# Kernel tuning notes

Measured on AMD Instinct MI355X. Metric: run time of the kernel, lower is better.

The kernel has to match this reference:

```python
import jax, jax.numpy as jnp
import numpy as np

NUM_EMBEDDINGS = 1024
EMBEDDING_DIM = 256
COMMITMENT_COST = 0.25
DECAY = 0.99
EPSILON = 1e-05


def setup_inputs() -> dict:
    key = jax.random.key(0)
    k1, k2, k3 = jax.random.split(key, 3)
    z = jax.random.normal(k1, (32, EMBEDDING_DIM, 32, 32), dtype=jnp.float32)
    codebook = jax.random.normal(k2, (NUM_EMBEDDINGS, EMBEDDING_DIM), dtype=jnp.float32)
    ema_cluster_size = jnp.zeros((NUM_EMBEDDINGS,), dtype=jnp.float32)
    ema_dw = jax.random.normal(k3, (NUM_EMBEDDINGS, EMBEDDING_DIM), dtype=jnp.float32)
    return {"z": z, "codebook": codebook, "ema_cluster_size": ema_cluster_size, "ema_dw": ema_dw}


def reference(z, codebook, ema_cluster_size, ema_dw):
    K, D = codebook.shape
    # (B,C,H,W) -> (B,H,W,C)
    zp = jnp.transpose(z, (0, 2, 3, 1))
    z_flat = zp.reshape(-1, D)  # [N, D]
    N = z_flat.shape[0]

    # squared L2 distances to each code: [N, K]
    distances = (jnp.sum(z_flat ** 2, axis=1, keepdims=True)
                 + jnp.sum(codebook ** 2, axis=1)
                 - 2.0 * z_flat @ codebook.T)
    idx = jnp.argmin(distances, axis=1)  # [N]

    quantized = codebook[idx].reshape(zp.shape)  # [B,H,W,C]

    # training-mode EMA codebook update (one-hot scatter expressed as segment sums)
    counts = jax.ops.segment_sum(jnp.ones((N,), z_flat.dtype), idx, num_segments=K)  # encodings.sum(0)
    dw = jax.ops.segment_sum(z_flat, idx, num_segments=K)                            # encodings.T @ z_flat
    new_cluster_size = ema_cluster_size * DECAY + (1.0 - DECAY) * counts
    new_ema_dw = ema_dw * DECAY + (1.0 - DECAY) * dw
    n = jnp.sum(new_cluster_size)
    cluster_size = (new_cluster_size + EPSILON) / (n + K * EPSILON) * n
    new_codebook = new_ema_dw / cluster_size[:, None]

    commitment_loss = jnp.mean((zp - jax.lax.stop_gradient(quantized)) ** 2)
    loss = COMMITMENT_COST * commitment_loss

    # straight-through estimator
    quantized_st = zp + jax.lax.stop_gradient(quantized - zp)

    avg_probs = counts / N
    perplexity = jnp.exp(-jnp.sum(avg_probs * jnp.log(avg_probs + 1e-10)))

    quantized_out = jnp.transpose(quantized_st, (0, 3, 1, 2))  # back to (B,C,H,W)
    return (quantized_out, loss, perplexity, new_codebook, new_cluster_size, new_ema_dw)
```

## Files before the change

### kernel.cpp

```cpp
#include <hip/hip_runtime.h>
#include <cfloat>
#include <cstdint>

#define B_BATCH 32
#define D_DIM   256
#define HW      1024
#define N_POS   32768
#define K_CODES 1024
#define DECAY_F   0.99f
#define ONE_M_DECAY 0.01f
#define EPS_F   1e-5f

#define OUT_Q    0
#define OUT_LOSS 8388608
#define OUT_PERP 8388609
#define OUT_CB   8388610
#define OUT_NCS  8650754
#define OUT_EDW  8651778


#define WS_COUNTS  0
#define WS_ZNORM   4096
#define WS_BSUM    4100
#define WS_MEMSET  4104
#define WS_CBNORM  4352
#define WS_OFFS    8448
#define WS_CURSOR  12544
#define WS_IDX     16640
#define WS_SORTED  147712
#define WS_CBHI    278784
#define WS_CBLO    803072
#define WS_PART    1327360
#define WS_SCODE   3424512
#define WS_TOTAL   3555584

typedef short s16x8 __attribute__((ext_vector_type(8)));
typedef float f32x4 __attribute__((ext_vector_type(4)));
typedef unsigned long long u64;

__device__ __forceinline__ ushort f2bf_rne(float x) {
    uint u = __float_as_uint(x);
    uint r = (u + 0x7FFF + ((u >> 16) & 1)) >> 16;
    return (ushort)r;
}
__device__ __forceinline__ float bf2f(ushort h) {
    return __uint_as_float(((uint)h) << 16);
}

__device__ __forceinline__ void gload16(const void* g, void* l) {
    __builtin_amdgcn_global_load_lds(
        (const __attribute__((address_space(1))) unsigned*)(uintptr_t)g,
        (__attribute__((address_space(3))) unsigned*)(uintptr_t)l, 16, 0, 0);
}

__global__ __launch_bounds__(256) void prep_ztrans(const float* __restrict__ z,
                                                   const float* __restrict__ cb,
                                                   ushort* __restrict__ zhi,
                                                   ushort* __restrict__ zlo,
                                                   ushort* __restrict__ cbhi,
                                                   ushort* __restrict__ cblo,
                                                   float* __restrict__ cbnorm,
                                                   float* __restrict__ znorm_acc) {
    __shared__ float Zs[32][65];
    __shared__ float red[256];
    const int tid = threadIdx.x;

    if (blockIdx.x >= 512) {
        int wave = tid >> 6;
        int lane = tid & 63;
        int k = (blockIdx.x - 512) * 4 + wave;
        float4 v = *(const float4*)&cb[(size_t)k * D_DIM + lane * 4];
        ushort4 h, l;
        h.x = f2bf_rne(v.x); l.x = f2bf_rne(v.x - bf2f(h.x));
        h.y = f2bf_rne(v.y); l.y = f2bf_rne(v.y - bf2f(h.y));
        h.z = f2bf_rne(v.z); l.z = f2bf_rne(v.z - bf2f(h.z));
        h.w = f2bf_rne(v.w); l.w = f2bf_rne(v.w - bf2f(h.w));
        *(ushort4*)&cbhi[(size_t)k * D_DIM + lane * 4] = h;
        *(ushort4*)&cblo[(size_t)k * D_DIM + lane * 4] = l;
        float s = v.x * v.x + v.y * v.y + v.z * v.z + v.w * v.w;
        #pragma unroll
        for (int off = 32; off >= 1; off >>= 1) s += __shfl_xor(s, off);
        if (lane == 0) cbnorm[k] = s;
        return;
    }

    const int n0  = blockIdx.x * 64;
    const int b   = n0 >> 10;
    const int hw0 = n0 & 1023;
    const float* zb = z + (size_t)b * (D_DIM * HW) + hw0;

    const int zn = tid & 63;
    const int zdb = (tid >> 6) * 8;
    const int n  = tid >> 2;
    const int dq = tid & 3;
    float zsum = 0.f;

    for (int d0 = 0; d0 < D_DIM; d0 += 32) {
        __syncthreads();
        #pragma unroll
        for (int j = 0; j < 8; ++j)
            Zs[zdb + j][zn] = zb[(size_t)(d0 + zdb + j) * HW + zn];
        __syncthreads();
        s16x8 hv, lv;
        #pragma unroll
        for (int j = 0; j < 8; ++j) {
            float f = Zs[dq * 8 + j][n];
            zsum += f * f;
            ushort hb = f2bf_rne(f);
            ushort lb = f2bf_rne(f - bf2f(hb));
            hv[j] = (short)hb;
            lv[j] = (short)lb;
        }
        *(s16x8*)&zhi[(size_t)(n0 + n) * D_DIM + d0 + dq * 8] = hv;
        *(s16x8*)&zlo[(size_t)(n0 + n) * D_DIM + d0 + dq * 8] = lv;
    }
    red[tid] = zsum;
    __syncthreads();
    for (int s2 = 128; s2 >= 1; s2 >>= 1) {
        if (tid < s2) red[tid] += red[tid + s2];
        __syncthreads();
    }
    if (tid == 0) atomicAdd(znorm_acc, red[0]);
}

__global__ __launch_bounds__(256) void argmin_gemm(const ushort* __restrict__ cbhi,
                                                   const ushort* __restrict__ cblo,
                                                   const ushort* __restrict__ zhi,
                                                   const ushort* __restrict__ zlo,
                                                   const float* __restrict__ cbnorm,
                                                   u64* __restrict__ partial) {
    __shared__ ushort lds[16384];
    __shared__ u64 kred[128][2];

    const int tid  = threadIdx.x;
    const int wave = tid >> 6;
    const int lane = tid & 63;
    const int col  = lane & 15;
    const int lg   = lane >> 4;
    const int blk = blockIdx.x;
    const int mt = (blk >> 3) & 7;
    const int pt = (blk & 7) | ((blk >> 6) << 3);
    const int ch = wave & 1;
    const int ph = wave >> 1;

    const int r0  = tid >> 2;
    const int dch = (tid & 3) ^ ((r0 >> 1) & 3);
    const size_t eA0 = (size_t)(mt * 128 + r0) * D_DIM + dch * 8;
    const size_t eB0 = (size_t)(pt * 128 + r0) * D_DIM + dch * 8;
    const int ldsw = wave * 512;

    const int swz = (lg ^ ((col >> 1) & 3)) * 8;
    const int soffA = (ch * 64 + col) * 32 + swz;
    const int soffB = (ph * 64 + col) * 32 + swz;

    f32x4 acc[4][4];
    #pragma unroll
    for (int mi = 0; mi < 4; ++mi)
        #pragma unroll
        for (int ni = 0; ni < 4; ++ni) acc[mi][ni] = {0.f, 0.f, 0.f, 0.f};

    for (int s8 = 0; s8 < 8; ++s8) {
        const int d0 = s8 * 32;
        __syncthreads();
        gload16(cbhi + eA0 + d0,            &lds[0     + ldsw]);
        gload16(cbhi + eA0 + 64 * 256 + d0, &lds[2048  + ldsw]);
        gload16(cblo + eA0 + d0,            &lds[4096  + ldsw]);
        gload16(cblo + eA0 + 64 * 256 + d0, &lds[6144  + ldsw]);
        gload16(zhi  + eB0 + d0,            &lds[8192  + ldsw]);
        gload16(zhi  + eB0 + 64 * 256 + d0, &lds[10240 + ldsw]);
        gload16(zlo  + eB0 + d0,            &lds[12288 + ldsw]);
        gload16(zlo  + eB0 + 64 * 256 + d0, &lds[14336 + ldsw]);
        __syncthreads();

        s16x8 ah[4], al[4], bh[4], bl[4];
        #pragma unroll
        for (int mi = 0; mi < 4; ++mi) {
            int so = soffA + mi * 512;
            ah[mi] = *(const s16x8*)&lds[so];
            al[mi] = *(const s16x8*)&lds[4096 + so];
        }
        #pragma unroll
        for (int ni = 0; ni < 4; ++ni) {
            int so = soffB + ni * 512;
            bh[ni] = *(const s16x8*)&lds[8192 + so];
            bl[ni] = *(const s16x8*)&lds[12288 + so];
        }
        #pragma unroll
        for (int mi = 0; mi < 4; ++mi)
            #pragma unroll
            for (int ni = 0; ni < 4; ++ni) {
                acc[mi][ni] = __builtin_amdgcn_mfma_f32_16x16x32_bf16(ah[mi], bh[ni], acc[mi][ni], 0, 0, 0);
                acc[mi][ni] = __builtin_amdgcn_mfma_f32_16x16x32_bf16(ah[mi], bl[ni], acc[mi][ni], 0, 0, 0);
                acc[mi][ni] = __builtin_amdgcn_mfma_f32_16x16x32_bf16(al[mi], bh[ni], acc[mi][ni], 0, 0, 0);
            }
    }

    const int kbase = mt * 128 + ch * 64;
    u64 best[4] = {~0ull, ~0ull, ~0ull, ~0ull};
    #pragma unroll
    for (int mi = 0; mi < 4; ++mi) {
        float4 cn = *(const float4*)&cbnorm[kbase + mi * 16 + lg * 4];
        const float* cnp = (const float*)&cn;
        #pragma unroll
        for (int ni = 0; ni < 4; ++ni) {
            #pragma unroll
            for (int r = 0; r < 4; ++r) {
                float dist = cnp[r] - 2.f * acc[mi][ni][r];
                uint ub = __float_as_uint(dist);
                ub = ub ^ (uint)(((int)ub >> 31) | 0x80000000);
                u64 key = ((u64)ub << 32) | (uint)(kbase + mi * 16 + lg * 4 + r);
                if (key < best[ni]) best[ni] = key;
            }
        }
    }
    #pragma unroll
    for (int ni = 0; ni < 4; ++ni) {
        u64 o = __shfl_xor(best[ni], 16); if (o < best[ni]) best[ni] = o;
        o = __shfl_xor(best[ni], 32); if (o < best[ni]) best[ni] = o;
    }
    if (lane < 16) {
        #pragma unroll
        for (int ni = 0; ni < 4; ++ni)
            kred[ph * 64 + ni * 16 + lane][ch] = best[ni];
    }
    __syncthreads();
    if (tid < 128) {
        u64 a = kred[tid][0], b = kred[tid][1];
        partial[(size_t)(pt * 128 + tid) * 8 + mt] = a < b ? a : b;
    }
}

__global__ __launch_bounds__(256) void combine_kernel(const u64* __restrict__ partial,
                                                      int* __restrict__ idx,
                                                      float* __restrict__ counts,
                                                      float* __restrict__ bsum_acc) {
    __shared__ int hist[1024];
    __shared__ float red[256];
    const int tid = threadIdx.x;
    for (int j = tid; j < 1024; j += 256) hist[j] = 0;
    __syncthreads();
    int n = blockIdx.x * 256 + tid;
    const u64* p = partial + (size_t)n * 8;
    u64 m = p[0];
    #pragma unroll
    for (int j = 1; j < 8; ++j) { u64 v = p[j]; if (v < m) m = v; }
    int k = (int)(m & 1023u);
    idx[n] = k;
    atomicAdd(&hist[k], 1);
    uint ub = (uint)(m >> 32);
    uint u = (ub & 0x80000000u) ? (ub ^ 0x80000000u) : ~ub;
    red[tid] = __uint_as_float(u);
    __syncthreads();
    for (int s2 = 128; s2 >= 1; s2 >>= 1) {
        if (tid < s2) red[tid] += red[tid + s2];
        __syncthreads();
    }
    if (tid == 0) atomicAdd(bsum_acc, red[0]);
    for (int j = tid; j < 1024; j += 256) {
        int c = hist[j];
        if (c) atomicAdd(&counts[j], (float)c);
    }
}

__global__ __launch_bounds__(1024) void small_kernel(const float* __restrict__ ema_cs,
                                                     const float* __restrict__ counts,
                                                     const float* __restrict__ znorm,
                                                     const float* __restrict__ bsum,
                                                     float* __restrict__ out_ncs,
                                                     float* __restrict__ out_perp,
                                                     float* __restrict__ out_loss,
                                                     float* __restrict__ ntot_ws,
                                                     int* __restrict__ offsets,
                                                     int* __restrict__ cursor) {
    __shared__ float s1[1024];
    __shared__ float s2[1024];
    __shared__ int   s3[1024];
    int k = threadIdx.x;
    float cnt = counts[k];
    float ncs = ema_cs[k] * DECAY_F + ONE_M_DECAY * cnt;
    out_ncs[k] = ncs;
    float p = cnt / (float)N_POS;
    s1[k] = ncs;
    s2[k] = p * logf(p + 1e-10f);
    int c = (int)cnt;
    s3[k] = c;
    __syncthreads();
    for (int off = 1; off < 1024; off <<= 1) {
        int v = (k >= off) ? s3[k - off] : 0;
        __syncthreads();
        s3[k] += v;
        __syncthreads();
    }
    int excl = s3[k] - c;
    offsets[k] = excl;
    cursor[k] = excl;
    for (int st = 512; st >= 1; st >>= 1) {
        if (k < st) { s1[k] += s1[k + st]; s2[k] += s2[k + st]; }
        __syncthreads();
    }
    if (k == 0) {
        ntot_ws[0] = s1[0];
        out_perp[0] = expf(-s2[0]);
        out_loss[0] = 0.25f * (znorm[0] + bsum[0]) / 8388608.0f;
    }
}

__global__ __launch_bounds__(256) void scatter_kernel(const int* __restrict__ idx,
                                                      int* __restrict__ cursor,
                                                      int* __restrict__ sorted,
                                                      int* __restrict__ scode,
                                                      float* __restrict__ dw_zero) {
    __shared__ int hist[1024];
    __shared__ int base_s[1024];
    const int tid = threadIdx.x;
    {
        float4 z4 = {0.f, 0.f, 0.f, 0.f};
        size_t e = ((size_t)blockIdx.x * 256 + tid) * 8;
        *(float4*)&dw_zero[e] = z4;
        *(float4*)&dw_zero[e + 4] = z4;
    }
    for (int j = tid; j < 1024; j += 256) hist[j] = 0;
    __syncthreads();
    int n = blockIdx.x * 256 + tid;
    int k = idx[n];
    atomicAdd(&hist[k], 1);
    __syncthreads();
    for (int j = tid; j < 1024; j += 256) {
        int c = hist[j];
        if (c) base_s[j] = atomicAdd(&cursor[j], c);
        hist[j] = 0;
    }
    __syncthreads();
    int rank = atomicAdd(&hist[k], 1);
    int pos = base_s[k] + rank;
    sorted[pos] = n;
    scode[pos] = k;
}

#define DW_CHUNK 64
__global__ __launch_bounds__(256) void dw_chunk_kernel(const ushort* __restrict__ zhi,
                                                       const ushort* __restrict__ zlo,
                                                       const int* __restrict__ sorted,
                                                       const int* __restrict__ scode,
                                                       const int* __restrict__ offsets,
                                                       const float* __restrict__ counts,
                                                       float* __restrict__ dw) {
    __shared__ int sid[DW_CHUNK];
    __shared__ int sk[DW_CHUNK];
    const int tid = threadIdx.x;
    const int p0 = blockIdx.x * DW_CHUNK;
    if (tid < DW_CHUNK) {
        sid[tid] = sorted[p0 + tid];
        sk[tid]  = scode[p0 + tid];
    }
    __syncthreads();
    float acc = 0.f;
    int runstart = 0;
    #pragma unroll 4
    for (int i = 0; i < DW_CHUNK; ++i) {
        int id = sid[i];
        float zv = bf2f(zhi[(size_t)id * D_DIM + tid]) + bf2f(zlo[(size_t)id * D_DIM + tid]);
        acc += zv;
        bool end = (i == DW_CHUNK - 1) || (sk[i + 1] != sk[i]);
        if (end) {
            int k = sk[i];
            int off = offsets[k];
            int cnt = (int)counts[k];
            if (p0 + runstart == off && p0 + i == off + cnt - 1)
                dw[(size_t)k * D_DIM + tid] = acc;
            else
                atomicAdd(&dw[(size_t)k * D_DIM + tid], acc);
            acc = 0.f;
            runstart = i + 1;
        }
    }
}

__global__ __launch_bounds__(256) void fuse_lite(const float* __restrict__ cb,
                                                 const int* __restrict__ idx,
                                                 float* __restrict__ outq) {
    __shared__ float Qs[32][65];
    __shared__ int kidx[64];
    const int tid = threadIdx.x;
    const int n0  = blockIdx.x * 64;
    const int b   = n0 >> 10;
    const int hw0 = n0 & 1023;
    float* ob = outq + (size_t)b * (D_DIM * HW) + hw0;

    if (tid < 64) kidx[tid] = idx[n0 + tid];

    for (int d0 = 0; d0 < D_DIM; d0 += 32) {
        __syncthreads();
        #pragma unroll
        for (int h = 0; h < 2; ++h) {
            int s  = tid + 256 * h;
            int n  = s >> 3;
            int dq = s & 7;
            int k  = kidx[n];
            float4 q = *(const float4*)&cb[(size_t)k * D_DIM + d0 + dq * 4];
            Qs[dq * 4 + 0][n] = q.x;
            Qs[dq * 4 + 1][n] = q.y;
            Qs[dq * 4 + 2][n] = q.z;
            Qs[dq * 4 + 3][n] = q.w;
        }
        __syncthreads();
        #pragma unroll
        for (int j = 0; j < 8; ++j) {
            int v = tid + 256 * j;
            int d = v >> 6;
            int n = v & 63;
            ob[(size_t)(d0 + d) * HW + n] = Qs[d][n];
        }
    }
}

__global__ __launch_bounds__(256) void finalize_rows(const float* __restrict__ ema_dw,
                                                     const float* __restrict__ out_ncs,
                                                     const float* __restrict__ ntot_ws,
                                                     float* __restrict__ out_edw,
                                                     float* __restrict__ out_cb) {
    int k = blockIdx.x;
    int d = threadIdx.x;
    float ncs = out_ncs[k];
    float nt = ntot_ws[0];
    float csz = (ncs + EPS_F) / (nt + (float)K_CODES * EPS_F) * nt;
    size_t e = (size_t)k * D_DIM + d;
    float ed = ema_dw[e] * DECAY_F + ONE_M_DECAY * out_edw[e];
    out_edw[e] = ed;
    out_cb[e] = ed / csz;
}

extern "C" void kernel_launch(void* const* d_in, const int* in_sizes, int n_in,
                              void* d_out, int out_size, void* d_ws, size_t ws_size,
                              hipStream_t stream) {
    const float* z       = (const float*)d_in[0];
    const float* cb      = (const float*)d_in[1];
    const float* ema_cs  = (const float*)d_in[2];
    const float* ema_dw  = (const float*)d_in[3];
    float* out = (float*)d_out;

    char* ws = (char*)d_ws;
    float* ws_counts = (float*)(ws + WS_COUNTS);
    float* ws_znorm  = (float*)(ws + WS_ZNORM);
    float* ws_bsum   = (float*)(ws + WS_BSUM);
    float* ws_cbnorm = (float*)(ws + WS_CBNORM);
    int*   ws_offs   = (int*)(ws + WS_OFFS);
    int*   ws_cursor = (int*)(ws + WS_CURSOR);
    int*   ws_idx    = (int*)(ws + WS_IDX);
    int*   ws_sorted = (int*)(ws + WS_SORTED);
    ushort* ws_cbhi  = (ushort*)(ws + WS_CBHI);
    ushort* ws_cblo  = (ushort*)(ws + WS_CBLO);
    u64*   ws_part   = (u64*)(ws + WS_PART);
    int*   ws_scode  = (int*)(ws + WS_SCODE);

    ushort* zhi = (ushort*)out;
    ushort* zlo = zhi + 8388608;

    hipMemsetAsync(d_ws, 0, WS_MEMSET, stream);

    prep_ztrans<<<768, 256, 0, stream>>>(z, cb, zhi, zlo, ws_cbhi, ws_cblo,
                                         ws_cbnorm, ws_znorm);
    argmin_gemm<<<2048, 256, 0, stream>>>(ws_cbhi, ws_cblo, zhi, zlo, ws_cbnorm, ws_part);
    combine_kernel<<<N_POS / 256, 256, 0, stream>>>(ws_part, ws_idx, ws_counts, ws_bsum);
    small_kernel<<<1, 1024, 0, stream>>>(ema_cs, ws_counts, ws_znorm, ws_bsum,
                                         out + OUT_NCS, out + OUT_PERP, out + OUT_LOSS,
                                         (float*)(ws + WS_ZNORM) + 1024, ws_offs, ws_cursor);
    scatter_kernel<<<N_POS / 256, 256, 0, stream>>>(ws_idx, ws_cursor, ws_sorted,
                                                    ws_scode, out + OUT_EDW);
    dw_chunk_kernel<<<N_POS / DW_CHUNK, 256, 0, stream>>>(zhi, zlo, ws_sorted, ws_scode,
                                                          ws_offs, ws_counts, out + OUT_EDW);
    fuse_lite<<<N_POS / 64, 256, 0, stream>>>(cb, ws_idx, out + OUT_Q);
    finalize_rows<<<K_CODES, 256, 0, stream>>>(ema_dw, out + OUT_NCS,
                                               (float*)(ws + WS_ZNORM) + 1024,
                                               out + OUT_EDW, out + OUT_CB);
}
```

Before: 213.9 us.

## Fuse combine and stats into argmin GEMM via last-block tickets; merge tail kernels

Folds the argmin combine step and the single-block statistics/prefix-sum kernel into the GEMM kernel. Atomic ticket counters let the last-arriving block per position tile do the combine, and the very last block compute the scan, perplexity and loss. The quantize-output kernel and the codebook finalize kernel are merged into one launch by block index. This removes three kernel launches and their serialization gaps, at the cost of extra threadfences and atomics plus a serial tail executed by a single block inside the GEMM.

Measured after the change: 453.4 us. +111.9%, slower.

```diff
diff --git a/kernel.cpp b/kernel.cpp
--- a/kernel.cpp
+++ b/kernel.cpp
@@ -22,17 +22,20 @@
 #define WS_COUNTS  0
 #define WS_ZNORM   4096
 #define WS_BSUM    4100
-#define WS_MEMSET  4104
-#define WS_CBNORM  4352
-#define WS_OFFS    8448
-#define WS_CURSOR  12544
-#define WS_IDX     16640
-#define WS_SORTED  147712
-#define WS_CBHI    278784
-#define WS_CBLO    803072
-#define WS_PART    1327360
-#define WS_SCODE   3424512
-#define WS_TOTAL   3555584
+#define WS_DONE    4104
+#define WS_NTOT    4108
+#define WS_TICKET  4112
+#define WS_MEMSET  5136
+#define WS_CBNORM  5376
+#define WS_OFFS    9472
+#define WS_CURSOR  13568
+#define WS_IDX     17664
+#define WS_SORTED  148736
+#define WS_CBHI    279808
+#define WS_CBLO    804096
+#define WS_PART    1328384
+#define WS_SCODE   3425536
+#define WS_TOTAL   3556608
 
 typedef short s16x8 __attribute__((ext_vector_type(8)));
 typedef float f32x4 __attribute__((ext_vector_type(4)));
@@ -128,9 +131,23 @@
                                                    const ushort* __restrict__ zhi,
                                                    const ushort* __restrict__ zlo,
                                                    const float* __restrict__ cbnorm,
-                                                   u64* __restrict__ partial) {
+                                                   u64* __restrict__ partial,
+                                                   int* __restrict__ ticket,
+                                                   int* __restrict__ done_ctr,
+                                                   int* __restrict__ idx,
+                                                   float* __restrict__ counts,
+                                                   float* __restrict__ bsum_acc,
+                                                   const float* __restrict__ znorm,
+                                                   const float* __restrict__ ema_cs,
+                                                   float* __restrict__ out_ncs,
+                                                   float* __restrict__ out_perp,
+                                                   float* __restrict__ out_loss,
+                                                   float* __restrict__ ntot_ws,
+                                                   int* __restrict__ offsets,
+                                                   int* __restrict__ cursor) {
     __shared__ ushort lds[16384];
     __shared__ u64 kred[128][2];
+    __shared__ int s_last, s_vlast;
 
     const int tid  = threadIdx.x;
     const int wave = tid >> 6;
@@ -228,80 +245,96 @@
         u64 a = kred[tid][0], b = kred[tid][1];
         partial[(size_t)(pt * 128 + tid) * 8 + mt] = a < b ? a : b;
     }
-}
-
-__global__ __launch_bounds__(256) void combine_kernel(const u64* __restrict__ partial,
-                                                      int* __restrict__ idx,
-                                                      float* __restrict__ counts,
-                                                      float* __restrict__ bsum_acc) {
-    __shared__ int hist[1024];
-    __shared__ float red[256];
-    const int tid = threadIdx.x;
+
+    __threadfence();
+    __syncthreads();
+    if (tid == 0) s_last = (atomicAdd(&ticket[pt], 1) == 7);
+    __syncthreads();
+    if (!s_last) return;
+
+    __threadfence();
+    int* hist = (int*)lds;
+    float* redf = (float*)((char*)lds + 4096);
     for (int j = tid; j < 1024; j += 256) hist[j] = 0;
     __syncthreads();
-    int n = blockIdx.x * 256 + tid;
-    const u64* p = partial + (size_t)n * 8;
-    u64 m = p[0];
-    #pragma unroll
-    for (int j = 1; j < 8; ++j) { u64 v = p[j]; if (v < m) m = v; }
-    int k = (int)(m & 1023u);
-    idx[n] = k;
-    atomicAdd(&hist[k], 1);
-    uint ub = (uint)(m >> 32);
-    uint u = (ub & 0x80000000u) ? (ub ^ 0x80000000u) : ~ub;
-    red[tid] = __uint_as_float(u);
+    float bd = 0.f;
+    if (tid < 128) {
+        int n = pt * 128 + tid;
+        const u64* p = partial + (size_t)n * 8;
+        u64 m = p[0];
+        #pragma unroll
+        for (int j = 1; j < 8; ++j) { u64 v = p[j]; if (v < m) m = v; }
+        int k = (int)(m & 1023u);
+        idx[n] = k;
+        atomicAdd(&hist[k], 1);
+        uint ub = (uint)(m >> 32);
+        uint u = (ub & 0x80000000u) ? (ub ^ 0x80000000u) : ~ub;
+        bd = __uint_as_float(u);
+    }
+    redf[tid] = bd;
     __syncthreads();
     for (int s2 = 128; s2 >= 1; s2 >>= 1) {
-        if (tid < s2) red[tid] += red[tid + s2];
-        __syncthreads();
-    }
-    if (tid == 0) atomicAdd(bsum_acc, red[0]);
+        if (tid < s2) redf[tid] += redf[tid + s2];
+        __syncthreads();
+    }
+    if (tid == 0) atomicAdd(bsum_acc, redf[0]);
     for (int j = tid; j < 1024; j += 256) {
         int c = hist[j];
         if (c) atomicAdd(&counts[j], (float)c);
     }
-}
-
-__global__ __launch_bounds__(1024) void small_kernel(const float* __restrict__ ema_cs,
-                                                     const float* __restrict__ counts,
-                                                     const float* __restrict__ znorm,
-                                                     const float* __restrict__ bsum,
-                                                     float* __restrict__ out_ncs,
-                                                     float* __restrict__ out_perp,
-                                                     float* __restrict__ out_loss,
-                                                     float* __restrict__ ntot_ws,
-                                                     int* __restrict__ offsets,
-                                                     int* __restrict__ cursor) {
-    __shared__ float s1[1024];
-    __shared__ float s2[1024];
-    __shared__ int   s3[1024];
-    int k = threadIdx.x;
-    float cnt = counts[k];
-    float ncs = ema_cs[k] * DECAY_F + ONE_M_DECAY * cnt;
-    out_ncs[k] = ncs;
-    float p = cnt / (float)N_POS;
-    s1[k] = ncs;
-    s2[k] = p * logf(p + 1e-10f);
-    int c = (int)cnt;
-    s3[k] = c;
-    __syncthreads();
-    for (int off = 1; off < 1024; off <<= 1) {
-        int v = (k >= off) ? s3[k - off] : 0;
-        __syncthreads();
-        s3[k] += v;
-        __syncthreads();
-    }
-    int excl = s3[k] - c;
-    offsets[k] = excl;
-    cursor[k] = excl;
-    for (int st = 512; st >= 1; st >>= 1) {
-        if (k < st) { s1[k] += s1[k + st]; s2[k] += s2[k + st]; }
-        __syncthreads();
-    }
-    if (k == 0) {
+
+    __threadfence();
+    __syncthreads();
+    if (tid == 0) s_vlast = (atomicAdd(done_ctr, 1) == 255);
+    __syncthreads();
+    if (!s_vlast) return;
+
+    __threadfence();
+    int*   si = (int*)lds;
+    float* s1 = (float*)((char*)lds + 4096);
+    float* s2 = (float*)((char*)lds + 5120);
+    const int base = tid * 4;
+    int c4[4];
+    int ssum = 0;
+    float n1 = 0.f, n2 = 0.f;
+    #pragma unroll
+    for (int j = 0; j < 4; ++j) {
+        float cnt = counts[base + j];
+        int ci = (int)cnt;
+        c4[j] = ci;
+        ssum += ci;
+        float ncs = ema_cs[base + j] * DECAY_F + ONE_M_DECAY * cnt;
+        out_ncs[base + j] = ncs;
+        n1 += ncs;
+        float p = cnt / (float)N_POS;
+        n2 += p * logf(p + 1e-10f);
+    }
+    si[tid] = ssum;
+    __syncthreads();
+    for (int off = 1; off < 256; off <<= 1) {
+        int v = (tid >= off) ? si[tid - off] : 0;
+        __syncthreads();
+        si[tid] += v;
+        __syncthreads();
+    }
+    int run = si[tid] - ssum;
+    #pragma unroll
+    for (int j = 0; j < 4; ++j) {
+        offsets[base + j] = run;
+        cursor[base + j] = run;
+        run += c4[j];
+    }
+    s1[tid] = n1;
+    s2[tid] = n2;
+    __syncthreads();
+    for (int st = 128; st >= 1; st >>= 1) {
+        if (tid < st) { s1[tid] += s1[tid + st]; s2[tid] += s2[tid + st]; }
+        __syncthreads();
+    }
+    if (tid == 0) {
         ntot_ws[0] = s1[0];
         out_perp[0] = expf(-s2[0]);
-        out_loss[0] = 0.25f * (znorm[0] + bsum[0]) / 8388608.0f;
+        out_loss[0] = 0.25f * (znorm[0] + bsum_acc[0]) / 8388608.0f;
     }
 }
 
@@ -376,13 +409,31 @@
     }
 }
 
-__global__ __launch_bounds__(256) void fuse_lite(const float* __restrict__ cb,
-                                                 const int* __restrict__ idx,
-                                                 float* __restrict__ outq) {
+__global__ __launch_bounds__(256) void tail_kernel(const float* __restrict__ cb,
+                                                   const int* __restrict__ idx,
+                                                   const float* __restrict__ ema_dw,
+                                                   const float* __restrict__ out_ncs,
+                                                   const float* __restrict__ ntot_ws,
+                                                   float* __restrict__ out_edw,
+                                                   float* __restrict__ out_cb,
+                                                   float* __restrict__ outq) {
     __shared__ float Qs[32][65];
     __shared__ int kidx[64];
     const int tid = threadIdx.x;
-    const int n0  = blockIdx.x * 64;
+
+    if (blockIdx.x < 1024) {
+        int k = blockIdx.x;
+        float ncs = out_ncs[k];
+        float nt = ntot_ws[0];
+        float csz = (ncs + EPS_F) / (nt + (float)K_CODES * EPS_F) * nt;
+        size_t e = (size_t)k * D_DIM + tid;
+        float ed = ema_dw[e] * DECAY_F + ONE_M_DECAY * out_edw[e];
+        out_edw[e] = ed;
+        out_cb[e] = ed / csz;
+        return;
+    }
+
+    const int n0  = (blockIdx.x - 1024) * 64;
     const int b   = n0 >> 10;
     const int hw0 = n0 & 1023;
     float* ob = outq + (size_t)b * (D_DIM * HW) + hw0;
@@ -414,22 +465,6 @@
     }
 }
 
-__global__ __launch_bounds__(256) void finalize_rows(const float* __restrict__ ema_dw,
-                                                     const float* __restrict__ out_ncs,
-                                                     const float* __restrict__ ntot_ws,
-                                                     float* __restrict__ out_edw,
-                                                     float* __restrict__ out_cb) {
-    int k = blockIdx.x;
-    int d = threadIdx.x;
-    float ncs = out_ncs[k];
-    float nt = ntot_ws[0];
-    float csz = (ncs + EPS_F) / (nt + (float)K_CODES * EPS_F) * nt;
-    size_t e = (size_t)k * D_DIM + d;
-    float ed = ema_dw[e] * DECAY_F + ONE_M_DECAY * out_edw[e];
-    out_edw[e] = ed;
-    out_cb[e] = ed / csz;
-}
-
 extern "C" void kernel_launch(void* const* d_in, const int* in_sizes, int n_in,
                               void* d_out, int out_size, void* d_ws, size_t ws_size,
                               hipStream_t stream) {
@@ -443,6 +478,9 @@
     float* ws_counts = (float*)(ws + WS_COUNTS);
     float* ws_znorm  = (float*)(ws + WS_ZNORM);
     float* ws_bsum   = (float*)(ws + WS_BSUM);
+    int*   ws_done   = (int*)(ws + WS_DONE);
+    float* ws_ntot   = (float*)(ws + WS_NTOT);
+    int*   ws_ticket = (int*)(ws + WS_TICKET);
     float* ws_cbnorm = (float*)(ws + WS_CBNORM);
     int*   ws_offs   = (int*)(ws + WS_OFFS);
     int*   ws_cursor = (int*)(ws + WS_CURSOR);
@@ -460,17 +498,15 @@
 
     prep_ztrans<<<768, 256, 0, stream>>>(z, cb, zhi, zlo, ws_cbhi, ws_cblo,
                                          ws_cbnorm, ws_znorm);
-    argmin_gemm<<<2048, 256, 0, stream>>>(ws_cbhi, ws_cblo, zhi, zlo, ws_cbnorm, ws_part);
-    combine_kernel<<<N_POS / 256, 256, 0, stream>>>(ws_part, ws_idx, ws_counts, ws_bsum);
-    small_kernel<<<1, 1024, 0, stream>>>(ema_cs, ws_counts, ws_znorm, ws_bsum,
-                                         out + OUT_NCS, out + OUT_PERP, out + OUT_LOSS,
-                                         (float*)(ws + WS_ZNORM) + 1024, ws_offs, ws_cursor);
+    argmin_gemm<<<2048, 256, 0, stream>>>(ws_cbhi, ws_cblo, zhi, zlo, ws_cbnorm,
+                                          ws_part, ws_ticket, ws_done,
+                                          ws_idx, ws_counts, ws_bsum, ws_znorm,
+                                          ema_cs, out + OUT_NCS, out + OUT_PERP,
+                                          out + OUT_LOSS, ws_ntot, ws_offs, ws_cursor);
     scatter_kernel<<<N_POS / 256, 256, 0, stream>>>(ws_idx, ws_cursor, ws_sorted,
                                                     ws_scode, out + OUT_EDW);
     dw_chunk_kernel<<<N_POS / DW_CHUNK, 256, 0, stream>>>(zhi, zlo, ws_sorted, ws_scode,
                                                           ws_offs, ws_counts, out + OUT_EDW);
-    fuse_lite<<<N_POS / 64, 256, 0, stream>>>(cb, ws_idx, out + OUT_Q);
-    finalize_rows<<<K_CODES, 256, 0, stream>>>(ema_dw, out + OUT_NCS,
-                                               (float*)(ws + WS_ZNORM) + 1024,
-                                               out + OUT_EDW, out + OUT_CB);
-}
+    tail_kernel<<<1536, 256, 0, stream>>>(cb, ws_idx, ema_dw, out + OUT_NCS, ws_ntot,
+                                          out + OUT_EDW, out + OUT_CB, out + OUT_Q);
+}
```
